# Optimization experiments

Hardware: AMD Instinct MI355X
Metric: run time of the kernel (lower is better)

## Reference

```python
import jax, jax.numpy as jnp
import numpy as np


def _rope(xh, theta_factor):
    # xh: [H, S, Dqk]; rotate first half against second half (as in source)
    S, D = xh.shape[-2], xh.shape[-1]
    d_rope = D // 2
    rate = theta_factor * (-jnp.arange(0, d_rope, dtype=xh.dtype) / d_rope)
    pos = jnp.arange(0, S, dtype=xh.dtype)
    rot = pos[:, None] * rate[None, :]            # [S, d_rope]
    sin, cos = jnp.sin(rot), jnp.cos(rot)
    x1, x2 = xh[..., :d_rope], xh[..., d_rope:]
    y1 = cos * x1 - sin * x2
    y2 = sin * x1 + cos * x2
    return jnp.concatenate([y1, y2], axis=-1)


def _mha(x, y, q, k, v, o, theta_factor):
    S = x.shape[0]
    d_model = x.shape[1]
    x_scale = 1.0 / jnp.sqrt(jnp.array(x.shape[1], x.dtype))
    y_scale = 1.0 / jnp.sqrt(jnp.array(y.shape[1], x.dtype))
    # causal additive mask: 0 on/below diagonal, -1e9 above
    mask = (jnp.tril(jnp.ones((S, S), x.dtype)) - 1.0) * 1000000000.0
    # per-head projections (note: source uses x_scale for both q and k)
    pre_q = jnp.einsum('sd,hdk->hsk', x, q) * x_scale
    pre_k = jnp.einsum('td,hdk->htk', y, k) * x_scale
    vs = jnp.einsum('td,hdv->htv', y, v) * y_scale
    rq = _rope(pre_q, theta_factor)
    rk = _rope(pre_k, theta_factor)
    attn_scale = 1.0 / jnp.sqrt(jnp.array(rq.shape[-1], x.dtype))
    scores = jnp.einsum('hsk,htk->hst', rq, rk) * attn_scale + mask
    w = jax.nn.softmax(scores, axis=-1)           # [H, S, S]
    z = jnp.einsum('hst,htv->hsv', w, vs)         # [H, S, Dv]
    out_scale = 1.0 / jnp.sqrt(jnp.array(o.shape[0] * o.shape[1], x.dtype))
    return jnp.einsum('hsv,hvd->sd', z, o) * out_scale


def setup_inputs() -> dict:
    key = jax.random.key(0)
    ks = jax.random.split(key, 5)
    S, D, H, Dqk, Dv = 2048, 2048, 16, 128, 128
    return {
        'x': jax.random.normal(ks[0], (S, D), jnp.float32),
        'q': jax.random.normal(ks[1], (H, D, Dqk), jnp.float32),
        'k': jax.random.normal(ks[2], (H, D, Dqk), jnp.float32),
        'v': jax.random.normal(ks[3], (H, D, Dv), jnp.float32),
        'o': jax.random.normal(ks[4], (H, Dv, D), jnp.float32),
        'theta_factor': jnp.array(10000.0, jnp.float32),
    }


def reference(x, q, k, v, o, theta_factor):
    # self-attention path (y = x), scale = 1
    return _mha(x, x, q, k, v, o, theta_factor)
```

## Files before the change

kernel.cpp:

```cpp
#include <hip/hip_runtime.h>


#define S_LEN   2048
#define D_MODEL 2048
#define NHEAD   16
#define DHEAD   128

using f32x4   = __attribute__((ext_vector_type(4))) float;
using f32x16  = __attribute__((ext_vector_type(16))) float;
using bf16x8  = __attribute__((ext_vector_type(8))) __bf16;

__device__ __forceinline__ unsigned short f2bf(float f) {
  unsigned int u = __builtin_bit_cast(unsigned int, f);
  u += 0x7fffu + ((u >> 16) & 1u);
  return (unsigned short)(u >> 16);
}
__device__ __forceinline__ int chunks_of(int qt) { return (4 * qt + 13) / 10; }

__device__ __forceinline__ void gl_lds16(const unsigned short* g, char* l) {
  __builtin_amdgcn_global_load_lds(
      (const __attribute__((address_space(1))) unsigned int*)g,
      (__attribute__((address_space(3))) unsigned int*)l, 16, 0, 0);
}

__global__ __launch_bounds__(256) void k_prep(
    const float* __restrict__ x, const float* __restrict__ q,
    const float* __restrict__ k, const float* __restrict__ v,
    const float* __restrict__ o, const float* __restrict__ theta_p,
    unsigned short* __restrict__ xb, unsigned short* __restrict__ wT,
    unsigned short* __restrict__ obT, float* __restrict__ sint,
    float* __restrict__ cost) {
  __shared__ float t[32][33];
  const int bid = blockIdx.x, tid = threadIdx.x;
  if (bid < 4096) {
    int i = (bid * 256 + tid) * 4;
    float4 vv = *reinterpret_cast<const float4*>(x + i);
    ushort4 ov; ov.x = f2bf(vv.x); ov.y = f2bf(vv.y); ov.z = f2bf(vv.z); ov.w = f2bf(vv.w);
    *reinterpret_cast<ushort4*>(xb + i) = ov;
  } else if (bid < 4608) {
    int i = (bid - 4096) * 256 + tid;
    int s = i >> 6, c = i & 63;
    float rate = theta_p[0] * (-(float)c / 64.0f);
    float sn, cs;
    sincosf((float)s * rate, &sn, &cs);
    sint[i] = sn; cost[i] = cs;
  } else {
    int ti = bid - 4608;
    int which = ti >> 12, i = ti & 4095;
    const float* ip; unsigned short* op; int C, b, rt, ct;
    const int R = 2048;
    if (which < 3) {
      C = 128; b = i >> 8; rt = (i >> 2) & 63; ct = i & 3;
      const float* src = which == 0 ? q : (which == 1 ? k : v);
      ip = src + (size_t)b * R * C;
      op = wT + (size_t)which * 4194304 + (size_t)b * R * C;
    } else {
      C = 2048; rt = i >> 6; ct = i & 63;
      ip = o; op = obT;
    }
    int tx = tid & 31, ty = tid >> 5;
    #pragma unroll
    for (int j = 0; j < 4; j++)
      t[ty + j * 8][tx] = ip[(size_t)(rt * 32 + ty + j * 8) * C + ct * 32 + tx];
    __syncthreads();
    #pragma unroll
    for (int j = 0; j < 4; j++)
      op[(size_t)(ct * 32 + ty + j * 8) * R + rt * 32 + tx] = f2bf(t[tx][ty + j * 8]);
  }
}

__global__ __launch_bounds__(256) void k_proj2(
    const unsigned short* __restrict__ xb, const unsigned short* __restrict__ wT,
    const float* __restrict__ sint, const float* __restrict__ cost,
    unsigned short* __restrict__ rq, unsigned short* __restrict__ rk,
    unsigned short* __restrict__ vst) {
  __shared__ char lds[32768];
  const int tid = threadIdx.x, l = tid & 63, w = tid >> 6;
  const int lr = l & 15, lk = l >> 4;
  const int orig = blockIdx.x;
  const int wg = (orig & 7) * 96 + (orig >> 3);
  const int bx = wg & 15, by = wg >> 4;
  const int s0 = bx * 128;
  const int h = by & 15, which = by >> 4;
  const unsigned short* bbase = wT + (size_t)by * 128 * D_MODEL;

  f32x4 acc[2][8] = {};

  auto stage = [&](int t, int buf) {
    const int kt = t * 32;
    char* dst = lds + buf * 16384;
    #pragma unroll
    for (int j = 0; j < 2; j++) {
      int ci = tid + j * 256;
      int r = ci >> 2, c4 = ci & 3;
      int csrc = (c4 ^ ((r >> 1) & 3)) * 8;
      gl_lds16(xb + (size_t)(s0 + r) * D_MODEL + kt + csrc, dst + ci * 16);
      gl_lds16(bbase + (size_t)r * D_MODEL + kt + csrc, dst + 8192 + ci * 16);
    }
  };

  stage(0, 0);
  int cur = 0;
  const int nT = D_MODEL / 32;
  for (int t = 0; t < nT; t++) {
    if (t + 1 < nT) {
      stage(t + 1, cur ^ 1);
      asm volatile("s_waitcnt vmcnt(4)" ::: "memory");
    } else {
      asm volatile("s_waitcnt vmcnt(0)" ::: "memory");
    }
    __builtin_amdgcn_s_barrier();
    const char* base = lds + cur * 16384;
    bf16x8 a[2], b[8];
    #pragma unroll
    for (int mf = 0; mf < 2; mf++) {
      int rr = w * 32 + mf * 16 + lr;
      a[mf] = *reinterpret_cast<const bf16x8*>(base + rr * 64 + ((lk ^ ((rr >> 1) & 3)) * 16));
    }
    #pragma unroll
    for (int nf = 0; nf < 8; nf++) {
      int rn = nf * 16 + lr;
      b[nf] = *reinterpret_cast<const bf16x8*>(base + 8192 + rn * 64 + ((lk ^ ((rn >> 1) & 3)) * 16));
    }
    #pragma unroll
    for (int mf = 0; mf < 2; mf++)
      #pragma unroll
      for (int nf = 0; nf < 8; nf++)
        acc[mf][nf] = __builtin_amdgcn_mfma_f32_16x16x32_bf16(a[mf], b[nf], acc[mf][nf], 0, 0, 0);
    asm volatile("s_waitcnt lgkmcnt(0)" ::: "memory");
    __builtin_amdgcn_s_barrier();
    cur ^= 1;
  }

  const float xscale = 0.022097086912079608f;
  const float qsc = xscale * 0.08838834764831845f;
  if (which < 2) {
    const float sc_out = (which == 0) ? qsc : xscale;
    unsigned short* dst = (which == 0 ? rq : rk) + (size_t)h * S_LEN * DHEAD;
    #pragma unroll
    for (int mf = 0; mf < 2; mf++) {
      #pragma unroll
      for (int nf = 0; nf < 4; nf++) {
        int c1 = nf * 16 + lr;
        #pragma unroll
        for (int rg = 0; rg < 4; rg++) {
          int srow = s0 + w * 32 + mf * 16 + lk * 4 + rg;
          float sn = sint[srow * 64 + c1], cs = cost[srow * 64 + c1];
          float x1 = acc[mf][nf][rg] * sc_out;
          float x2 = acc[mf][nf + 4][rg] * sc_out;
          dst[(size_t)srow * DHEAD + c1]      = f2bf(cs * x1 - sn * x2);
          dst[(size_t)srow * DHEAD + c1 + 64] = f2bf(sn * x1 + cs * x2);
        }
      }
    }
  } else {
    unsigned short* dst = vst + (size_t)h * DHEAD * S_LEN;
    #pragma unroll
    for (int mf = 0; mf < 2; mf++) {
      int rbase = s0 + w * 32 + mf * 16 + lk * 4;
      #pragma unroll
      for (int nf = 0; nf < 8; nf++) {
        int c = nf * 16 + lr;
        ushort4 ov;
        ov.x = f2bf(acc[mf][nf][0] * xscale); ov.y = f2bf(acc[mf][nf][1] * xscale);
        ov.z = f2bf(acc[mf][nf][2] * xscale); ov.w = f2bf(acc[mf][nf][3] * xscale);
        *reinterpret_cast<ushort4*>(dst + (size_t)c * S_LEN + rbase) = ov;
      }
    }
  }
}

__global__ __launch_bounds__(256, 2) void k_attn6(
    const unsigned short* __restrict__ rq, const unsigned short* __restrict__ rk,
    const unsigned short* __restrict__ vst,
    unsigned short* __restrict__ opart, float2* __restrict__ mlbuf) {
  __shared__ uint4 ldsbuf[2368];
  char* lds = (char*)ldsbuf;
  const int tid = threadIdx.x, l = tid & 63, w = tid >> 6;
  const int hi = l >> 5, qcol = l & 31;
  const int b = blockIdx.x;
  const int h = b & 15;
  int u = b >> 4, qt = 0;
  while (u >= chunks_of(qt)) { u -= chunks_of(qt); qt++; }
  const int ntile = 4 * qt + 4;
  const int tbeg = u * 10;
  const int tend = (tbeg + 10 < ntile) ? tbeg + 10 : ntile;
  const int s0w = qt * 128 + w * 32;
  const int wlast = s0w + 31;
  const int dtile = s0w >> 5;

  const unsigned short* rk_h  = rk  + (size_t)h * S_LEN * DHEAD;
  const unsigned short* vst_h = vst + (size_t)h * DHEAD * S_LEN;

  const unsigned short* qrow_p = rq + ((size_t)h * S_LEN + s0w + qcol) * DHEAD + hi * 8;
  bf16x8 qb[8];
  #pragma unroll
  for (int kk = 0; kk < 8; kk++)
    qb[kk] = *reinterpret_cast<const bf16x8*>(qrow_p + kk * 16);

  f32x16 O[4] = {};
  float mrow = -3.0e38f, lrow = 0.0f;

  uint4 kreg[2], vreg[2];
  auto ld_regs = [&](int t) {
    const int t0 = t * 32;
    #pragma unroll
    for (int j = 0; j < 2; j++) {
      int ci = tid + j * 256;
      kreg[j] = *reinterpret_cast<const uint4*>(rk_h + (size_t)(t0 + (ci >> 4)) * DHEAD + (ci & 15) * 8);
      vreg[j] = *reinterpret_cast<const uint4*>(vst_h + (size_t)(ci >> 2) * S_LEN + t0 + (ci & 3) * 8);
    }
  };
  auto wr_lds = [&](int p) {
    char* dst = lds + p * 18944;
    #pragma unroll
    for (int j = 0; j < 2; j++) {
      int ci = tid + j * 256;
      *reinterpret_cast<uint4*>(dst + (ci >> 4) * 272 + (ci & 15) * 16) = kreg[j];
      *reinterpret_cast<uint4*>(dst + 8704 + (ci >> 2) * 80 + (ci & 3) * 16) = vreg[j];
    }
  };

  ld_regs(tbeg);
  wr_lds(0);
  if (tbeg + 1 < tend) ld_regs(tbeg + 1);
  asm volatile("s_waitcnt lgkmcnt(0)" ::: "memory");
  __builtin_amdgcn_s_barrier();

  int cur = 0;
  for (int t = tbeg; t < tend; t++) {
    const char* kb = lds + cur * 18944;
    const char* vb = kb + 8704;
    const int tt0 = t * 32;
    if (tt0 <= wlast) {
      f32x16 sc = {};
      #pragma unroll
      for (int kk = 0; kk < 8; kk++) {
        bf16x8 ka = *reinterpret_cast<const bf16x8*>(kb + qcol * 272 + kk * 32 + hi * 16);
        sc = __builtin_amdgcn_mfma_f32_32x32x16_bf16(ka, qb[kk], sc, 0, 0, 0);
      }
      float p[16];
      #pragma unroll
      for (int r = 0; r < 16; r++) p[r] = sc[r];
      if (t == dtile) {
        #pragma unroll
        for (int r = 0; r < 16; r++)
          if (((r & 3) + 8 * (r >> 2) + 4 * hi) > qcol) p[r] = -1.0e9f;
      }
      float mx[8];
      #pragma unroll
      for (int i = 0; i < 8; i++) mx[i] = fmaxf(p[2 * i], p[2 * i + 1]);
      #pragma unroll
      for (int i = 0; i < 4; i++) mx[i] = fmaxf(mx[i], mx[i + 4]);
      mx[0] = fmaxf(mx[0], mx[2]); mx[1] = fmaxf(mx[1], mx[3]);
      float pmax = fmaxf(mx[0], mx[1]);
      pmax = fmaxf(pmax, __shfl_xor(pmax, 32, 64));
      if (__any(pmax > mrow + 8.0f)) {
        float mn = fmaxf(mrow, pmax);
        float sf = __expf(mrow - mn);
        lrow *= sf; mrow = mn;
        #pragma unroll
        for (int vc = 0; vc < 4; vc++)
          #pragma unroll
          for (int r = 0; r < 16; r++) O[vc][r] *= sf;
      }
      #pragma unroll
      for (int r = 0; r < 16; r++) p[r] = __expf(p[r] - mrow);
      float sm[8];
      #pragma unroll
      for (int i = 0; i < 8; i++) sm[i] = p[2 * i] + p[2 * i + 1];
      #pragma unroll
      for (int i = 0; i < 4; i++) sm[i] += sm[i + 4];
      float psum = (sm[0] + sm[1]) + (sm[2] + sm[3]);
      psum += __shfl_xor(psum, 32, 64);
      lrow += psum;
      unsigned int pk[2][4], sw[2][4];
      #pragma unroll
      for (int c = 0; c < 2; c++)
        #pragma unroll
        for (int k = 0; k < 4; k++) {
          unsigned int r_;
          asm("v_cvt_pk_bf16_f32 %0, %1, %2" : "=v"(r_)
              : "v"(p[8 * c + 2 * k]), "v"(p[8 * c + 2 * k + 1]));
          pk[c][k] = r_;
          sw[c][k] = (unsigned int)__shfl_xor((int)r_, 32, 64);
        }
      bf16x8 pb[2];
      #pragma unroll
      for (int c = 0; c < 2; c++) {
        union { unsigned int u4[4]; bf16x8 v; } bw;
        bw.u4[0] = hi ? sw[c][2] : pk[c][0];
        bw.u4[1] = hi ? sw[c][3] : pk[c][1];
        bw.u4[2] = hi ? pk[c][2] : sw[c][0];
        bw.u4[3] = hi ? pk[c][3] : sw[c][1];
        pb[c] = bw.v;
      }
      #pragma unroll
      for (int vc = 0; vc < 4; vc++) {
        const char* vrow = vb + (vc * 32 + qcol) * 80 + hi * 16;
        bf16x8 va0 = *reinterpret_cast<const bf16x8*>(vrow);
        bf16x8 va1 = *reinterpret_cast<const bf16x8*>(vrow + 32);
        O[vc] = __builtin_amdgcn_mfma_f32_32x32x16_bf16(va0, pb[0], O[vc], 0, 0, 0);
        O[vc] = __builtin_amdgcn_mfma_f32_32x32x16_bf16(va1, pb[1], O[vc], 0, 0, 0);
      }
    }
    if (t + 1 < tend) {
      wr_lds(cur ^ 1);
      if (t + 2 < tend) ld_regs(t + 2);
    }
    asm volatile("s_waitcnt lgkmcnt(0)" ::: "memory");
    __builtin_amdgcn_s_barrier();
    cur ^= 1;
  }

  __syncthreads();
  float inv = lrow > 0.0f ? 1.0f / lrow : 0.0f;
  #pragma unroll
  for (int vc = 0; vc < 4; vc++)
    #pragma unroll
    for (int g = 0; g < 4; g++) {
      int v0 = vc * 32 + 8 * g + 4 * hi;
      ushort4 ov;
      ov.x = f2bf(O[vc][4 * g + 0] * inv); ov.y = f2bf(O[vc][4 * g + 1] * inv);
      ov.z = f2bf(O[vc][4 * g + 2] * inv); ov.w = f2bf(O[vc][4 * g + 3] * inv);
      *reinterpret_cast<ushort4*>(lds + (w * 32 + qcol) * 272 + v0 * 2) = ov;
    }
  __syncthreads();
  #pragma unroll
  for (int j = 0; j < 8; j++) {
    int row = w * 32 + j * 4 + (l >> 4);
    uint4 vv = *reinterpret_cast<const uint4*>(lds + row * 272 + (l & 15) * 16);
    *reinterpret_cast<uint4*>(opart + ((size_t)b * 128 + row) * DHEAD + (l & 15) * 8) = vv;
  }
  if (l < 32)
    mlbuf[(size_t)b * 128 + w * 32 + l] = make_float2(mrow, lrow);
}

__global__ void k_comb2(const unsigned short* __restrict__ opart,
                        const float2* __restrict__ mlbuf,
                        unsigned short* __restrict__ z) {
  int g = blockIdx.x * 256 + threadIdx.x;
  int vg = g & 15, q = (g >> 4) & 2047, h = g >> 15;
  int qt = q >> 7, r = q & 127;
  int base = 0;
  for (int j = 0; j < qt; j++) base += chunks_of(j);
  const int nc = chunks_of(qt);
  float m = -3.0e38f;
  float2 ml[7];
  #pragma unroll
  for (int cc = 0; cc < 7; cc++)
    if (cc < nc) {
      ml[cc] = mlbuf[(size_t)((base + cc) * 16 + h) * 128 + r];
      m = fmaxf(m, ml[cc].x);
    }
  float wts[7], wsum = 0.0f;
  #pragma unroll
  for (int cc = 0; cc < 7; cc++)
    if (cc < nc) {
      float wv = ml[cc].y > 0.0f ? ml[cc].y * __expf(ml[cc].x - m) : 0.0f;
      wts[cc] = wv; wsum += wv;
    }
  float wi = 1.0f / wsum;
  float acc[8] = {};
  #pragma unroll
  for (int cc = 0; cc < 7; cc++)
    if (cc < nc && wts[cc] > 0.0f) {
      float wv = wts[cc] * wi;
      bf16x8 v = *reinterpret_cast<const bf16x8*>(
          opart + ((size_t)((base + cc) * 16 + h) * 128 + r) * DHEAD + vg * 8);
      #pragma unroll
      for (int j = 0; j < 8; j++) acc[j] += wv * (float)v[j];
    }
  unsigned short* zp = z + (size_t)q * D_MODEL + h * DHEAD + vg * 8;
  ushort4 lo, hi4;
  lo.x = f2bf(acc[0]); lo.y = f2bf(acc[1]); lo.z = f2bf(acc[2]); lo.w = f2bf(acc[3]);
  hi4.x = f2bf(acc[4]); hi4.y = f2bf(acc[5]); hi4.z = f2bf(acc[6]); hi4.w = f2bf(acc[7]);
  *reinterpret_cast<ushort4*>(zp) = lo;
  *reinterpret_cast<ushort4*>(zp + 4) = hi4;
}

__global__ __launch_bounds__(256) void k_out2(
    const unsigned short* __restrict__ zb, const unsigned short* __restrict__ obT,
    float* __restrict__ out) {
  __shared__ char lds[49152];
  const int tid = threadIdx.x, l = tid & 63, w = tid >> 6;
  const int lr = l & 15, lk = l >> 4;
  const int orig = blockIdx.x;
  const int wg = (orig & 7) * 64 + (orig >> 3);
  const int bx = wg & 31, by = wg >> 5;
  const int s0 = bx * 64, n0 = by * 128;
  const int wm = w >> 1, wn = w & 1;
  f32x4 acc[2][4] = {};

  auto stage = [&](int t, int buf) {
    const int kt = t * 64;
    char* dst = lds + buf * 24576;
    #pragma unroll
    for (int j = 0; j < 2; j++) {
      int ci = tid + j * 256;
      int r = ci >> 3, c8 = ci & 7;
      int csrc = (c8 ^ (r & 7)) * 8;
      gl_lds16(zb + (size_t)(s0 + r) * D_MODEL + kt + csrc, dst + ci * 16);
    }
    #pragma unroll
    for (int j = 0; j < 4; j++) {
      int ci = tid + j * 256;
      int r = ci >> 3, c8 = ci & 7;
      int csrc = (c8 ^ (r & 7)) * 8;
      gl_lds16(obT + (size_t)(n0 + r) * D_MODEL + kt + csrc, dst + 8192 + ci * 16);
    }
  };

  stage(0, 0);
  int cur = 0;
  const int nT = D_MODEL / 64;
  for (int t = 0; t < nT; t++) {
    if (t + 1 < nT) {
      stage(t + 1, cur ^ 1);
      asm volatile("s_waitcnt vmcnt(6)" ::: "memory");
    } else {
      asm volatile("s_waitcnt vmcnt(0)" ::: "memory");
    }
    __builtin_amdgcn_s_barrier();
    const char* base = lds + cur * 24576;
    #pragma unroll
    for (int kk = 0; kk < 2; kk++) {
      const int kb = kk * 64 + lk * 16;
      bf16x8 a[2], b[4];
      #pragma unroll
      for (int mf = 0; mf < 2; mf++) {
        int rr = wm * 32 + mf * 16 + lr;
        a[mf] = *reinterpret_cast<const bf16x8*>(base + rr * 128 + (kb ^ ((rr & 7) << 4)));
      }
      #pragma unroll
      for (int nf = 0; nf < 4; nf++) {
        int rn = wn * 64 + nf * 16 + lr;
        b[nf] = *reinterpret_cast<const bf16x8*>(base + 8192 + rn * 128 + (kb ^ ((rn & 7) << 4)));
      }
      #pragma unroll
      for (int mf = 0; mf < 2; mf++)
        #pragma unroll
        for (int nf = 0; nf < 4; nf++)
          acc[mf][nf] = __builtin_amdgcn_mfma_f32_16x16x32_bf16(a[mf], b[nf], acc[mf][nf], 0, 0, 0);
    }
    asm volatile("s_waitcnt lgkmcnt(0)" ::: "memory");
    __builtin_amdgcn_s_barrier();
    cur ^= 1;
  }
  const float osc = 0.022097086912079608f;
  #pragma unroll
  for (int mf = 0; mf < 2; mf++)
    #pragma unroll
    for (int nf = 0; nf < 4; nf++)
      #pragma unroll
      for (int rg = 0; rg < 4; rg++)
        out[(size_t)(s0 + wm * 32 + mf * 16 + lk * 4 + rg) * D_MODEL + n0 + wn * 64 + nf * 16 + lr]
            = acc[mf][nf][rg] * osc;
}

extern "C" void kernel_launch(void* const* d_in, const int* in_sizes, int n_in,
                              void* d_out, int out_size, void* d_ws, size_t ws_size,
                              hipStream_t stream) {
  const float* x = (const float*)d_in[0];
  const float* q = (const float*)d_in[1];
  const float* k = (const float*)d_in[2];
  const float* v = (const float*)d_in[3];
  const float* o = (const float*)d_in[4];
  const float* theta = (const float*)d_in[5];
  float* out = (float*)d_out;

  char* ws = (char*)d_ws;
  const size_t MB = 1u << 20;
  unsigned short* xb  = (unsigned short*)(ws + 0 * MB);
  unsigned short* qbT = (unsigned short*)(ws + 8 * MB);
  unsigned short* obT = (unsigned short*)(ws + 32 * MB);
  unsigned short* rq  = (unsigned short*)(ws + 40 * MB);
  unsigned short* rk  = (unsigned short*)(ws + 48 * MB);
  unsigned short* vst = (unsigned short*)(ws + 56 * MB);
  float* sint = (float*)(ws + 64 * MB);
  float* cost = (float*)(ws + 64 * MB + 512 * 1024);
  unsigned short* opart = (unsigned short*)(ws + 0 * MB);
  float2* mlbuf         = (float2*)(ws + 31 * MB);
  unsigned short* zb    = (unsigned short*)(ws + 40 * MB);

  k_prep<<<dim3(20992), dim3(256), 0, stream>>>(x, q, k, v, o, theta, xb, qbT, obT, sint, cost);
  k_proj2<<<dim3(768), dim3(256), 0, stream>>>(xb, qbT, sint, cost, rq, rk, vst);
  k_attn6<<<dim3(976), dim3(256), 0, stream>>>(rq, rk, vst, opart, mlbuf);
  k_comb2<<<dim3(2048), dim3(256), 0, stream>>>(opart, mlbuf, zb);
  k_out2<<<dim3(512), dim3(256), 0, stream>>>(zb, obT, out);
}
```

Measured before the change: 180.4 us.

## Enlarge QKV projection GEMM tile to 256x256 with 8 waves and deeper K staging

New measurement: 183.3 us. About the same (+1.6%).

```diff
diff --git a/kernel.cpp b/kernel.cpp
--- a/kernel.cpp
+++ b/kernel.cpp
@@ -69,67 +69,88 @@
   }
 }
 
-__global__ __launch_bounds__(256) void k_proj2(
+__global__ __launch_bounds__(512) void k_proj3(
     const unsigned short* __restrict__ xb, const unsigned short* __restrict__ wT,
     const float* __restrict__ sint, const float* __restrict__ cost,
     unsigned short* __restrict__ rq, unsigned short* __restrict__ rk,
     unsigned short* __restrict__ vst) {
-  __shared__ char lds[32768];
+  __shared__ char lds[131072];
   const int tid = threadIdx.x, l = tid & 63, w = tid >> 6;
   const int lr = l & 15, lk = l >> 4;
+  const int wm = w >> 1, wn = w & 1;
   const int orig = blockIdx.x;
-  const int wg = (orig & 7) * 96 + (orig >> 3);
-  const int bx = wg & 15, by = wg >> 4;
-  const int s0 = bx * 128;
-  const int h = by & 15, which = by >> 4;
-  const unsigned short* bbase = wT + (size_t)by * 128 * D_MODEL;
-
-  f32x4 acc[2][8] = {};
+  const int wg = (orig & 7) * 24 + (orig >> 3);
+  const int bx = wg & 7, by = wg >> 3;
+  const int s0 = bx * 256;
+  const int panel = by * 2 + wn;
+  const int h = panel & 15, which = panel >> 4;
+  const unsigned short* bbase = wT + (size_t)by * 256 * D_MODEL;
+
+  f32x4 acc[4][8] = {};
 
   auto stage = [&](int t, int buf) {
-    const int kt = t * 32;
-    char* dst = lds + buf * 16384;
-    #pragma unroll
-    for (int j = 0; j < 2; j++) {
-      int ci = tid + j * 256;
-      int r = ci >> 2, c4 = ci & 3;
-      int csrc = (c4 ^ ((r >> 1) & 3)) * 8;
+    const int kt = t * 64;
+    char* dst = lds + buf * 65536;
+    #pragma unroll
+    for (int j = 0; j < 4; j++) {
+      int ci = j * 512 + tid;
+      int r = ci >> 3, c8 = ci & 7;
+      int csrc = (c8 ^ (r & 7)) * 8;
       gl_lds16(xb + (size_t)(s0 + r) * D_MODEL + kt + csrc, dst + ci * 16);
-      gl_lds16(bbase + (size_t)r * D_MODEL + kt + csrc, dst + 8192 + ci * 16);
+      gl_lds16(bbase + (size_t)r * D_MODEL + kt + csrc, dst + 32768 + ci * 16);
     }
   };
 
+  const int nT = D_MODEL / 64;
   stage(0, 0);
-  int cur = 0;
-  const int nT = D_MODEL / 32;
+  stage(1, 1);
+  asm volatile("s_waitcnt vmcnt(8)" ::: "memory");
+  __builtin_amdgcn_s_barrier();
+
   for (int t = 0; t < nT; t++) {
-    if (t + 1 < nT) {
-      stage(t + 1, cur ^ 1);
-      asm volatile("s_waitcnt vmcnt(4)" ::: "memory");
-    } else {
+    const char* base = lds + (t & 1) * 65536;
+    #pragma unroll
+    for (int p = 0; p < 4; p++) {
+      const int qm = p >> 1, qn = p & 1;
+      bf16x8 a[2][2], b[4][2];
+      #pragma unroll
+      for (int mi = 0; mi < 2; mi++) {
+        int rr = wm * 64 + (2 * qm + mi) * 16 + lr;
+        #pragma unroll
+        for (int ks = 0; ks < 2; ks++)
+          a[mi][ks] = *reinterpret_cast<const bf16x8*>(
+              base + rr * 128 + ((ks * 64 + lk * 16) ^ ((rr & 7) << 4)));
+      }
+      #pragma unroll
+      for (int ni = 0; ni < 4; ni++) {
+        int rn = wn * 128 + (4 * qn + ni) * 16 + lr;
+        #pragma unroll
+        for (int ks = 0; ks < 2; ks++)
+          b[ni][ks] = *reinterpret_cast<const bf16x8*>(
+              base + 32768 + rn * 128 + ((ks * 64 + lk * 16) ^ ((rn & 7) << 4)));
+      }
+      asm volatile("s_waitcnt lgkmcnt(0)" ::: "memory");
+      __builtin_amdgcn_sched_barrier(0);
+      __builtin_amdgcn_s_setprio(1);
+      #pragma unroll
+      for (int mi = 0; mi < 2; mi++)
+        #pragma unroll
+        for (int ni = 0; ni < 4; ni++)
+          #pragma unroll
+          for (int ks = 0; ks < 2; ks++)
+            acc[2 * qm + mi][4 * qn + ni] = __builtin_amdgcn_mfma_f32_16x16x32_bf16(
+                a[mi][ks], b[ni][ks], acc[2 * qm + mi][4 * qn + ni], 0, 0, 0);
+      __builtin_amdgcn_s_setprio(0);
+      __builtin_amdgcn_s_barrier();
+    }
+    if (t + 2 < nT) {
+      stage(t + 2, t & 1);
+      asm volatile("s_waitcnt vmcnt(8)" ::: "memory");
+      __builtin_amdgcn_s_barrier();
+    } else if (t + 1 < nT) {
       asm volatile("s_waitcnt vmcnt(0)" ::: "memory");
-    }
-    __builtin_amdgcn_s_barrier();
-    const char* base = lds + cur * 16384;
-    bf16x8 a[2], b[8];
-    #pragma unroll
-    for (int mf = 0; mf < 2; mf++) {
-      int rr = w * 32 + mf * 16 + lr;
-      a[mf] = *reinterpret_cast<const bf16x8*>(base + rr * 64 + ((lk ^ ((rr >> 1) & 3)) * 16));
-    }
-    #pragma unroll
-    for (int nf = 0; nf < 8; nf++) {
-      int rn = nf * 16 + lr;
-      b[nf] = *reinterpret_cast<const bf16x8*>(base + 8192 + rn * 64 + ((lk ^ ((rn >> 1) & 3)) * 16));
-    }
-    #pragma unroll
-    for (int mf = 0; mf < 2; mf++)
-      #pragma unroll
-      for (int nf = 0; nf < 8; nf++)
-        acc[mf][nf] = __builtin_amdgcn_mfma_f32_16x16x32_bf16(a[mf], b[nf], acc[mf][nf], 0, 0, 0);
-    asm volatile("s_waitcnt lgkmcnt(0)" ::: "memory");
-    __builtin_amdgcn_s_barrier();
-    cur ^= 1;
+      __builtin_amdgcn_s_barrier();
+    }
   }
 
   const float xscale = 0.022097086912079608f;
@@ -138,13 +159,13 @@
     const float sc_out = (which == 0) ? qsc : xscale;
     unsigned short* dst = (which == 0 ? rq : rk) + (size_t)h * S_LEN * DHEAD;
     #pragma unroll
-    for (int mf = 0; mf < 2; mf++) {
+    for (int mf = 0; mf < 4; mf++) {
       #pragma unroll
       for (int nf = 0; nf < 4; nf++) {
         int c1 = nf * 16 + lr;
         #pragma unroll
         for (int rg = 0; rg < 4; rg++) {
-          int srow = s0 + w * 32 + mf * 16 + lk * 4 + rg;
+          int srow = s0 + wm * 64 + mf * 16 + lk * 4 + rg;
           float sn = sint[srow * 64 + c1], cs = cost[srow * 64 + c1];
           float x1 = acc[mf][nf][rg] * sc_out;
           float x2 = acc[mf][nf + 4][rg] * sc_out;
@@ -156,8 +177,8 @@
   } else {
     unsigned short* dst = vst + (size_t)h * DHEAD * S_LEN;
     #pragma unroll
-    for (int mf = 0; mf < 2; mf++) {
-      int rbase = s0 + w * 32 + mf * 16 + lk * 4;
+    for (int mf = 0; mf < 4; mf++) {
+      int rbase = s0 + wm * 64 + mf * 16 + lk * 4;
       #pragma unroll
       for (int nf = 0; nf < 8; nf++) {
         int c = nf * 16 + lr;
@@ -484,7 +505,7 @@
   unsigned short* zb    = (unsigned short*)(ws + 40 * MB);
 
   k_prep<<<dim3(20992), dim3(256), 0, stream>>>(x, q, k, v, o, theta, xb, qbT, obT, sint, cost);
-  k_proj2<<<dim3(768), dim3(256), 0, stream>>>(xb, qbT, sint, cost, rq, rk, vst);
+  k_proj3<<<dim3(192), dim3(512), 0, stream>>>(xb, qbT, sint, cost, rq, rk, vst);
   k_attn6<<<dim3(976), dim3(256), 0, stream>>>(rq, rk, vst, opart, mlbuf);
   k_comb2<<<dim3(2048), dim3(256), 0, stream>>>(opart, mlbuf, zb);
   k_out2<<<dim3(512), dim3(256), 0, stream>>>(zb, obT, out);
```
